# Kernel tuning notes

Measured on AMD Instinct MI355X. Metric: run time of the kernel, lower is better.

The kernel has to match this reference:

```python
import jax, jax.numpy as jnp
import numpy as np

B, S, H, A = 16, 2048, 1024, 8


def setup_inputs() -> dict:
    key = jax.random.key(0)
    k1, k2, k3, k4 = jax.random.split(key, 4)
    token_embeddings = jax.random.normal(k1, (B, S, H), dtype=jnp.float32)
    aspect_embedding = jax.random.normal(k2, (B, A, H), dtype=jnp.float32)
    # Linear(2H -> H): stored as [2H, H] so we can use x @ W (same math as torch W^T)
    W = jax.random.normal(k3, (2 * H, H), dtype=jnp.float32) * (1.0 / np.sqrt(2 * H))
    b = jnp.zeros((H,), dtype=jnp.float32)
    v = jax.random.uniform(k4, (H,), dtype=jnp.float32)  # torch.rand init
    return {"token_embeddings": token_embeddings, "aspect_embedding": aspect_embedding,
            "W": W, "b": b, "v": v}


def reference(token_embeddings, aspect_embedding, W, b, v):
    # mean-pool aspect tokens -> [B, 1, H], broadcast over seq
    asp = jnp.mean(aspect_embedding, axis=1, keepdims=True)
    asp = jnp.broadcast_to(asp, token_embeddings.shape)          # [B, S, H]
    combined = jnp.concatenate([token_embeddings, asp], axis=2)   # [B, S, 2H]
    energy = jnp.tanh(combined @ W + b)                           # [B, S, H]
    scores = jnp.einsum('bsh,h->bs', energy, v)                   # [B, S]
    weights = jax.nn.softmax(scores, axis=1)                      # [B, S]
    # token * weights + token  ==  token * (1 + weights)
    return token_embeddings * (1.0 + weights[:, :, None])
```

## Files before the change

### kernel.cpp

```cpp
#include <hip/hip_runtime.h>
#include <hip/hip_bf16.h>
#include <stdint.h>


#define SEQ 2048
#define H 1024
#define MTOT 32768
#define BK 32

typedef __bf16 bf16x8 __attribute__((ext_vector_type(8)));
typedef float  f32x4  __attribute__((ext_vector_type(4)));

__device__ __forceinline__ void async16(const void* g, void* l) {
  __builtin_amdgcn_global_load_lds(
      (const __attribute__((address_space(1))) unsigned*)g,
      (__attribute__((address_space(3))) unsigned*)l, 16, 0, 0);
}

__device__ __forceinline__ unsigned f2bfraw(float f) {
  unsigned x = __float_as_uint(f);
  return (x + 0x7fffu + ((x >> 16) & 1u)) >> 16;
}
__device__ __forceinline__ float fast_tanh(float x) {
  x = fminf(fmaxf(x, -40.0f), 40.0f);
  float e = __expf(2.0f * x);
  return 1.0f - 2.0f / (e + 1.0f);
}

__global__ __launch_bounds__(256) void convert_tok(
    const float* __restrict__ in, unsigned short* __restrict__ ob) {
  const size_t i = ((size_t)blockIdx.x * 256 + threadIdx.x) * 8;
  const f32x4 a = *reinterpret_cast<const f32x4*>(in + i);
  const f32x4 b = *reinterpret_cast<const f32x4*>(in + i + 4);
  uint4 r;
  r.x = f2bfraw(a[0]) | (f2bfraw(a[1]) << 16);
  r.y = f2bfraw(a[2]) | (f2bfraw(a[3]) << 16);
  r.z = f2bfraw(b[0]) | (f2bfraw(b[1]) << 16);
  r.w = f2bfraw(b[2]) | (f2bfraw(b[3]) << 16);
  *reinterpret_cast<uint4*>(ob + i) = r;
}

__global__ __launch_bounds__(256) void transpose_w(
    const float* __restrict__ W, unsigned short* __restrict__ WT) {
  __shared__ float tile[32][33];
  const int x = threadIdx.x;
  const int y = threadIdx.y;
  const int n0 = blockIdx.x * 32, k0 = blockIdx.y * 32;
#pragma unroll
  for (int i = 0; i < 4; ++i)
    tile[y + 8 * i][x] = W[(size_t)(k0 + y + 8 * i) * H + n0 + x];
  __syncthreads();
#pragma unroll
  for (int i = 0; i < 4; ++i)
    WT[(size_t)(n0 + y + 8 * i) * H + k0 + x] = (unsigned short)f2bfraw(tile[x][y + 8 * i]);
}

__global__ __launch_bounds__(256) void aspect_c(
    const float* __restrict__ asp,
    const float* __restrict__ W,
    const float* __restrict__ bias,
    float* __restrict__ c) {
  const int b = blockIdx.x, nc = blockIdx.y;
  const int t = threadIdx.x;
  __shared__ float am[H];
#pragma unroll
  for (int j = 0; j < 4; ++j) {
    const int k = t + 256 * j;
    float s = 0.f;
#pragma unroll
    for (int a = 0; a < 8; ++a) s += asp[(size_t)(b * 8 + a) * H + k];
    am[k] = s * 0.125f;
  }
  __syncthreads();
  const int n = nc * 256 + t;
  float acc = bias[n];
  for (int k = 0; k < H; ++k) acc += am[k] * W[(size_t)(H + k) * H + n];
  c[b * H + n] = acc;
}

__global__ __launch_bounds__(256) void gemm_score(
    const __hip_bfloat16* __restrict__ tokb,
    const __hip_bfloat16* __restrict__ wt,
    const float* __restrict__ c,
    const float* __restrict__ v,
    float* __restrict__ part) {
  __shared__ __hip_bfloat16 As[128 * BK];
  __shared__ __hip_bfloat16 Bs[128 * BK];
  const int t = threadIdx.x;
  const int lane = t & 63;
  const int w = t >> 6;
  const int wm = w >> 1, wn = w & 1;
  const int m0 = blockIdx.y * 128;
  const int n0 = blockIdx.x * 128;
  const int bb = blockIdx.y >> 4;

  f32x4 acc[4][4] = {};

  const int srow = t >> 2, scol = (t & 3) * 8;
  const __hip_bfloat16* ga = tokb + (size_t)(m0 + srow) * H + scol;
  const __hip_bfloat16* gb = wt + (size_t)(n0 + srow) * H + scol;
  __hip_bfloat16* la0 = As + t * 8;
  __hip_bfloat16* la1 = As + t * 8 + 64 * BK;
  __hip_bfloat16* lb0 = Bs + t * 8;
  __hip_bfloat16* lb1 = Bs + t * 8 + 64 * BK;

  const int quad = lane >> 4, l16 = lane & 15;

  for (int k0 = 0; k0 < H; k0 += BK) {
    __syncthreads();
    async16(ga + k0, la0);
    async16(ga + k0 + (size_t)64 * H, la1);
    async16(gb + k0, lb0);
    async16(gb + k0 + (size_t)64 * H, lb1);
    __syncthreads();

    bf16x8 af[4], bf[4];
#pragma unroll
    for (int mi = 0; mi < 4; ++mi)
      af[mi] = *reinterpret_cast<const bf16x8*>(
          As + (wm * 64 + mi * 16 + l16) * BK + quad * 8);
#pragma unroll
    for (int ni = 0; ni < 4; ++ni)
      bf[ni] = *reinterpret_cast<const bf16x8*>(
          Bs + (wn * 64 + ni * 16 + l16) * BK + quad * 8);
#pragma unroll
    for (int mi = 0; mi < 4; ++mi)
#pragma unroll
      for (int ni = 0; ni < 4; ++ni)
        acc[mi][ni] = __builtin_amdgcn_mfma_f32_16x16x32_bf16(
            af[mi], bf[ni], acc[mi][ni], 0, 0, 0);
  }

  float vv[4], cc[4];
#pragma unroll
  for (int ni = 0; ni < 4; ++ni) {
    const int gn = n0 + wn * 64 + ni * 16 + l16;
    vv[ni] = v[gn];
    cc[ni] = c[bb * H + gn];
  }
  const size_t pbase = ((size_t)blockIdx.x * 2 + wn) * MTOT + m0;
#pragma unroll
  for (int mi = 0; mi < 4; ++mi) {
#pragma unroll
    for (int r = 0; r < 4; ++r) {
      float s = 0.f;
#pragma unroll
      for (int ni = 0; ni < 4; ++ni)
        s += fast_tanh(acc[mi][ni][r] + cc[ni]) * vv[ni];
#pragma unroll
      for (int msk = 1; msk < 16; msk <<= 1) s += __shfl_xor(s, msk, 64);
      if (l16 == 0)
        part[pbase + wm * 64 + mi * 16 + quad * 4 + r] = s;
    }
  }
}

__global__ __launch_bounds__(256) void softmax_k(
    const float* __restrict__ part, float* __restrict__ wts) {
  const int b = blockIdx.x, t = threadIdx.x;
  const int lane = t & 63, w = t >> 6;
  __shared__ float sm[SEQ];
  __shared__ float red[4];
  for (int s = t; s < SEQ; s += 256) {
    float sc = 0.f;
#pragma unroll
    for (int p = 0; p < 16; ++p) sc += part[(size_t)p * MTOT + b * SEQ + s];
    sm[s] = sc;
  }
  __syncthreads();
  float m = -1e30f;
  for (int s = t; s < SEQ; s += 256) m = fmaxf(m, sm[s]);
#pragma unroll
  for (int o = 1; o < 64; o <<= 1) m = fmaxf(m, __shfl_xor(m, o, 64));
  if (lane == 0) red[w] = m;
  __syncthreads();
  m = fmaxf(fmaxf(red[0], red[1]), fmaxf(red[2], red[3]));
  __syncthreads();
  float sum = 0.f;
  for (int s = t; s < SEQ; s += 256) sum += __expf(sm[s] - m);
#pragma unroll
  for (int o = 1; o < 64; o <<= 1) sum += __shfl_xor(sum, o, 64);
  if (lane == 0) red[w] = sum;
  __syncthreads();
  sum = red[0] + red[1] + red[2] + red[3];
  const float inv = 1.0f / sum;
  for (int s = t; s < SEQ; s += 256)
    wts[(size_t)b * SEQ + s] = __expf(sm[s] - m) * inv;
}

__global__ __launch_bounds__(256) void scale_k(
    const float* __restrict__ tok, const float* __restrict__ wts,
    float* __restrict__ out) {
  const size_t i = ((size_t)blockIdx.x * 256 + threadIdx.x) * 4;
  const float wm = 1.0f + wts[i >> 10];
  const f32x4 a = *reinterpret_cast<const f32x4*>(tok + i);
  f32x4 o;
  o[0] = a[0] * wm; o[1] = a[1] * wm; o[2] = a[2] * wm; o[3] = a[3] * wm;
  *reinterpret_cast<f32x4*>(out + i) = o;
}

extern "C" void kernel_launch(void* const* d_in, const int* in_sizes, int n_in,
                              void* d_out, int out_size, void* d_ws, size_t ws_size,
                              hipStream_t stream) {
  const float* tok  = (const float*)d_in[0];
  const float* asp  = (const float*)d_in[1];
  const float* W    = (const float*)d_in[2];
  const float* bias = (const float*)d_in[3];
  const float* v    = (const float*)d_in[4];
  float* out = (float*)d_out;

  unsigned short* tokb_u = (unsigned short*)out;
  float*          c_buf  = out + 32489472;
  float*          part   = out + 32505856;
  unsigned short* WT_u   = (unsigned short*)(out + 33030144);
  float* wts = (ws_size >= (size_t)(SEQ * 16 * 4)) ? (float*)d_ws
                                                   : (float*)d_in[1];

  convert_tok<<<16384, 256, 0, stream>>>(tok, tokb_u);
  transpose_w<<<dim3(32, 32), dim3(32, 8), 0, stream>>>(W, WT_u);
  aspect_c<<<dim3(16, 4), 256, 0, stream>>>(asp, W, bias, c_buf);
  gemm_score<<<dim3(8, 256), 256, 0, stream>>>(
      (const __hip_bfloat16*)tokb_u, (const __hip_bfloat16*)WT_u,
      c_buf, v, part);
  softmax_k<<<16, 256, 0, stream>>>(part, wts);
  scale_k<<<32768, 256, 0, stream>>>(tok, wts, out);
}
```

Before: 445.3 us.

## Split aspect projection over K, swizzle GEMM blocks, widen softmax kernel

The aspect projection kernel is split over four K chunks with vectorized float4 weight loads and a per-block reduction. Its partial sums are written to a scratch region and summed inside the GEMM epilogue. This raises parallelism in what was a 64-block serial loop. The GEMM block index is remapped so consecutive blocks share the same N tile, which should improve L2 reuse of the weight tile. Softmax now uses 1024 threads holding scores in registers instead of shared memory, cutting its latency at the cost of four extra loads per column in the GEMM epilogue.

```diff
diff --git a/kernel.cpp b/kernel.cpp
--- a/kernel.cpp
+++ b/kernel.cpp
@@ -59,29 +59,51 @@
     const float* __restrict__ asp,
     const float* __restrict__ W,
     const float* __restrict__ bias,
-    float* __restrict__ c) {
-  const int b = blockIdx.x, nc = blockIdx.y;
+    float* __restrict__ cpart) {
+  const int b = blockIdx.x, nc = blockIdx.y, kc = blockIdx.z;
   const int t = threadIdx.x;
-  __shared__ float am[H];
-#pragma unroll
-  for (int j = 0; j < 4; ++j) {
-    const int k = t + 256 * j;
+  const int lane = t & 63, w = t >> 6;
+  __shared__ float am[256];
+  __shared__ f32x4 red[4][64];
+  {
+    const int k = kc * 256 + t;
     float s = 0.f;
 #pragma unroll
     for (int a = 0; a < 8; ++a) s += asp[(size_t)(b * 8 + a) * H + k];
-    am[k] = s * 0.125f;
-  }
-  __syncthreads();
-  const int n = nc * 256 + t;
-  float acc = bias[n];
-  for (int k = 0; k < H; ++k) acc += am[k] * W[(size_t)(H + k) * H + n];
-  c[b * H + n] = acc;
+    am[t] = s * 0.125f;
+  }
+  __syncthreads();
+  const int n = nc * 256 + lane * 4;
+  const float* wp = W + (size_t)(H + kc * 256 + w * 64) * H + n;
+  f32x4 acc = {};
+#pragma unroll 8
+  for (int k = 0; k < 64; ++k) {
+    const f32x4 wv = *reinterpret_cast<const f32x4*>(wp + (size_t)k * H);
+    const float a = am[w * 64 + k];
+    acc[0] += a * wv[0]; acc[1] += a * wv[1];
+    acc[2] += a * wv[2]; acc[3] += a * wv[3];
+  }
+  red[w][lane] = acc;
+  __syncthreads();
+  if (w == 0) {
+    f32x4 r = red[0][lane];
+#pragma unroll
+    for (int i = 1; i < 4; ++i) {
+      const f32x4 x = red[i][lane];
+      r[0] += x[0]; r[1] += x[1]; r[2] += x[2]; r[3] += x[3];
+    }
+    if (kc == 0) {
+      r[0] += bias[n];     r[1] += bias[n + 1];
+      r[2] += bias[n + 2]; r[3] += bias[n + 3];
+    }
+    *reinterpret_cast<f32x4*>(cpart + (size_t)kc * 16 * H + b * H + n) = r;
+  }
 }
 
 __global__ __launch_bounds__(256) void gemm_score(
     const __hip_bfloat16* __restrict__ tokb,
     const __hip_bfloat16* __restrict__ wt,
-    const float* __restrict__ c,
+    const float* __restrict__ cpart,
     const float* __restrict__ v,
     float* __restrict__ part) {
   __shared__ __hip_bfloat16 As[128 * BK];
@@ -90,9 +112,13 @@
   const int lane = t & 63;
   const int w = t >> 6;
   const int wm = w >> 1, wn = w & 1;
-  const int m0 = blockIdx.y * 128;
-  const int n0 = blockIdx.x * 128;
-  const int bb = blockIdx.y >> 4;
+  const unsigned bidl = blockIdx.x + (blockIdx.y << 3);
+  const unsigned nb = ((bidl & 7u) << 8) | (bidl >> 3);
+  const int bx = nb & 7;
+  const int by = nb >> 3;
+  const int m0 = by * 128;
+  const int n0 = bx * 128;
+  const int bb = by >> 4;
 
   f32x4 acc[4][4] = {};
 
@@ -136,9 +162,13 @@
   for (int ni = 0; ni < 4; ++ni) {
     const int gn = n0 + wn * 64 + ni * 16 + l16;
     vv[ni] = v[gn];
-    cc[ni] = c[bb * H + gn];
-  }
-  const size_t pbase = ((size_t)blockIdx.x * 2 + wn) * MTOT + m0;
+    float s = cpart[(size_t)bb * H + gn];
+    s += cpart[(size_t)1 * 16 * H + bb * H + gn];
+    s += cpart[(size_t)2 * 16 * H + bb * H + gn];
+    s += cpart[(size_t)3 * 16 * H + bb * H + gn];
+    cc[ni] = s;
+  }
+  const size_t pbase = ((size_t)bx * 2 + wn) * MTOT + m0;
 #pragma unroll
   for (int mi = 0; mi < 4; ++mi) {
 #pragma unroll
@@ -155,37 +185,40 @@
   }
 }
 
-__global__ __launch_bounds__(256) void softmax_k(
+__global__ __launch_bounds__(1024) void softmax_k(
     const float* __restrict__ part, float* __restrict__ wts) {
   const int b = blockIdx.x, t = threadIdx.x;
   const int lane = t & 63, w = t >> 6;
-  __shared__ float sm[SEQ];
-  __shared__ float red[4];
-  for (int s = t; s < SEQ; s += 256) {
-    float sc = 0.f;
-#pragma unroll
-    for (int p = 0; p < 16; ++p) sc += part[(size_t)p * MTOT + b * SEQ + s];
-    sm[s] = sc;
-  }
-  __syncthreads();
-  float m = -1e30f;
-  for (int s = t; s < SEQ; s += 256) m = fmaxf(m, sm[s]);
+  __shared__ float red[16];
+  const int s0 = t * 2;
+  float sx = 0.f, sy = 0.f;
+#pragma unroll
+  for (int p = 0; p < 16; ++p) {
+    const float2 x = *reinterpret_cast<const float2*>(
+        part + (size_t)p * MTOT + b * SEQ + s0);
+    sx += x.x; sy += x.y;
+  }
+  float m = fmaxf(sx, sy);
 #pragma unroll
   for (int o = 1; o < 64; o <<= 1) m = fmaxf(m, __shfl_xor(m, o, 64));
   if (lane == 0) red[w] = m;
   __syncthreads();
-  m = fmaxf(fmaxf(red[0], red[1]), fmaxf(red[2], red[3]));
-  __syncthreads();
-  float sum = 0.f;
-  for (int s = t; s < SEQ; s += 256) sum += __expf(sm[s] - m);
+  m = red[0];
+#pragma unroll
+  for (int i = 1; i < 16; ++i) m = fmaxf(m, red[i]);
+  __syncthreads();
+  const float e0 = __expf(sx - m), e1 = __expf(sy - m);
+  float sum = e0 + e1;
 #pragma unroll
   for (int o = 1; o < 64; o <<= 1) sum += __shfl_xor(sum, o, 64);
   if (lane == 0) red[w] = sum;
   __syncthreads();
-  sum = red[0] + red[1] + red[2] + red[3];
+  sum = 0.f;
+#pragma unroll
+  for (int i = 0; i < 16; ++i) sum += red[i];
   const float inv = 1.0f / sum;
-  for (int s = t; s < SEQ; s += 256)
-    wts[(size_t)b * SEQ + s] = __expf(sm[s] - m) * inv;
+  float2 o2; o2.x = e0 * inv; o2.y = e1 * inv;
+  *reinterpret_cast<float2*>(wts + (size_t)b * SEQ + s0) = o2;
 }
 
 __global__ __launch_bounds__(256) void scale_k(
@@ -210,7 +243,7 @@
   float* out = (float*)d_out;
 
   unsigned short* tokb_u = (unsigned short*)out;
-  float*          c_buf  = out + 32489472;
+  float*          cpart  = out + 16777216;
   float*          part   = out + 32505856;
   unsigned short* WT_u   = (unsigned short*)(out + 33030144);
   float* wts = (ws_size >= (size_t)(SEQ * 16 * 4)) ? (float*)d_ws
@@ -218,10 +251,10 @@
 
   convert_tok<<<16384, 256, 0, stream>>>(tok, tokb_u);
   transpose_w<<<dim3(32, 32), dim3(32, 8), 0, stream>>>(W, WT_u);
-  aspect_c<<<dim3(16, 4), 256, 0, stream>>>(asp, W, bias, c_buf);
+  aspect_c<<<dim3(16, 4, 4), 256, 0, stream>>>(asp, W, bias, cpart);
   gemm_score<<<dim3(8, 256), 256, 0, stream>>>(
       (const __hip_bfloat16*)tokb_u, (const __hip_bfloat16*)WT_u,
-      c_buf, v, part);
-  softmax_k<<<16, 256, 0, stream>>>(part, wts);
+      cpart, v, part);
+  softmax_k<<<16, 1024, 0, stream>>>(part, wts);
   scale_k<<<32768, 256, 0, stream>>>(tok, wts, out);
 }
```

Result: faster. 369.2 us (-17.1%).
